# Performance work log

Measured on AMD Instinct MI355X. Metric: run time of the kernel, lower is better.

The kernel has to match this reference:

```python
import jax, jax.numpy as jnp
import numpy as np

N0, N1, N2 = 200000, 100000, 20000
E1, E2 = 1600000, 320000
D_IN, D_H, D_OUT = 128, 256, 64


def _segment_mean(vals, seg_ids, num_segments):
    # vals: [E, D], seg_ids: [E] int -> [num_segments, D] mean over incoming edges
    sums = jax.ops.segment_sum(vals, seg_ids, num_segments=num_segments)
    cnt = jax.ops.segment_sum(jnp.ones((vals.shape[0],), vals.dtype), seg_ids,
                              num_segments=num_segments)
    return sums / jnp.maximum(cnt, 1.0)[:, None]


def setup_inputs() -> dict:
    key = jax.random.key(0)
    ks = jax.random.split(key, 9)
    s = 1.0 / np.sqrt(D_IN)
    s2 = 1.0 / np.sqrt(D_H)
    return {
        "x": jax.random.normal(ks[0], (N0, D_IN), jnp.float32),
        "src1": jax.random.randint(ks[1], (E1,), 0, N0, jnp.int32),
        "dst1": jax.random.randint(ks[2], (E1,), 0, N1, jnp.int32),
        "src2": jax.random.randint(ks[3], (E2,), 0, N1, jnp.int32),
        "dst2": jax.random.randint(ks[4], (E2,), 0, N2, jnp.int32),
        "W_l1": jax.random.uniform(ks[5], (D_H, D_IN), jnp.float32, -s, s),
        "b_l1": jnp.zeros((D_H,), jnp.float32),
        "W_r1": jax.random.uniform(ks[6], (D_H, D_IN), jnp.float32, -s, s),
        "W_l2": jax.random.uniform(ks[7], (D_OUT, D_H), jnp.float32, -s2, s2),
        "b_l2": jnp.zeros((D_OUT,), jnp.float32),
        "W_r2": jax.random.uniform(ks[8], (D_OUT, D_H), jnp.float32, -s2, s2),
    }


def reference(x, src1, dst1, src2, dst2, W_l1, b_l1, W_r1, W_l2, b_l2, W_r2):
    # Layer 1: bipartite SAGEConv (N0 sources -> N1 targets), mean aggregation
    agg1 = _segment_mean(x[src1], dst1, N1)                    # [N1, D_IN]
    h1 = agg1 @ W_l1.T + b_l1 + x[:N1] @ W_r1.T                # [N1, D_H]
    h1 = jax.nn.relu(h1)                                       # dropout: eval no-op
    # Layer 2: (N1 -> N2)
    agg2 = _segment_mean(h1[src2], dst2, N2)                   # [N2, D_H]
    h2 = agg2 @ W_l2.T + b_l2 + h1[:N2] @ W_r2.T               # [N2, D_OUT]
    return jax.nn.log_softmax(h2, axis=-1)
```

## Files before the change

### kernel.cpp

```cpp
#include <hip/hip_runtime.h>
#include <hip/hip_fp8.h>
#include <stdint.h>


#define CN0 200000
#define CN1 100000
#define CN2 20000
#define CE1 1600000
#define CE2 320000
#define CD_IN 128
#define CD_H 256
#define CD_OUT 64

#define NBK1 196
#define NBK2 40
#define G1 256
#define G2 64
#define CHUNK1 6250
#define CHUNK2 5000

typedef __bf16 bf16x8 __attribute__((ext_vector_type(8)));
typedef float f32x2 __attribute__((ext_vector_type(2)));
typedef float f32x4 __attribute__((ext_vector_type(4)));
typedef float f32x16 __attribute__((ext_vector_type(16)));
typedef uint16_t u16x4 __attribute__((ext_vector_type(4)));

__device__ inline uint16_t f2bf(float f) {
  uint32_t u = __float_as_uint(f);
  return (uint16_t)((u + 0x7fffu + ((u >> 16) & 1u)) >> 16);
}
__device__ inline float blo(uint32_t v) { return __uint_as_float(v << 16); }
__device__ inline float bhi(uint32_t v) { return __uint_as_float(v & 0xffff0000u); }

__device__ inline uint32_t f32x4_to_fp8x4(float a, float b, float c, float d) {
#if __has_builtin(__builtin_amdgcn_cvt_pk_fp8_f32)
  uint32_t pk = (uint32_t)__builtin_amdgcn_cvt_pk_fp8_f32(a, b, 0, false);
  pk = (uint32_t)__builtin_amdgcn_cvt_pk_fp8_f32(c, d, (int)pk, true);
  return pk;
#else
  __hip_fp8_e4m3 e0(a), e1(b), e2(c), e3(d);
  return (uint32_t)e0.__x | ((uint32_t)e1.__x << 8) |
         ((uint32_t)e2.__x << 16) | ((uint32_t)e3.__x << 24);
#endif
}

__device__ inline float fp8_one(uint32_t b) {
  uint32_t s = (b >> 7) & 1u, e = (b >> 3) & 15u, m = b & 7u;
  float f = (e == 0) ? (float)m * 0.001953125f
                     : __uint_as_float(((e + 120u) << 23) | (m << 20));
  return s ? -f : f;
}

__device__ inline void fp8x4_dec(uint32_t w, float& p0, float& p1,
                                 float& p2, float& p3) {
#if __has_builtin(__builtin_amdgcn_cvt_pk_f32_fp8)
  f32x2 lo = __builtin_amdgcn_cvt_pk_f32_fp8(w, false);
  f32x2 hi = __builtin_amdgcn_cvt_pk_f32_fp8(w, true);
  p0 = lo[0]; p1 = lo[1]; p2 = hi[0]; p3 = hi[1];
#else
  p0 = fp8_one(w & 0xffu);
  p1 = fp8_one((w >> 8) & 0xffu);
  p2 = fp8_one((w >> 16) & 0xffu);
  p3 = fp8_one((w >> 24) & 0xffu);
#endif
}

__device__ inline void fp8x4_acc(uint32_t w, float& p0, float& p1,
                                 float& p2, float& p3) {
  float q0, q1, q2, q3;
  fp8x4_dec(w, q0, q1, q2, q3);
  p0 += q0; p1 += q1; p2 += q2; p3 += q3;
}

__device__ inline bf16x8 fp8x8_to_bf16x8(uint2 v) {
  float f[8];
  fp8x4_dec(v.x, f[0], f[1], f[2], f[3]);
  fp8x4_dec(v.y, f[4], f[5], f[6], f[7]);
  uint16_t o[8];
#pragma unroll
  for (int e = 0; e < 8; ++e) o[e] = f2bf(f[e]);
  return *reinterpret_cast<bf16x8*>(o);
}

__global__ __launch_bounds__(256) void cvt_count(
    const float* __restrict__ x, const float* __restrict__ Wl1,
    const float* __restrict__ Wr1, const float* __restrict__ Wl2,
    const float* __restrict__ Wr2, const int* __restrict__ dst1,
    const int* __restrict__ dst2, uint32_t* __restrict__ x_fp8,
    uint16_t* __restrict__ wfragG, uint16_t* __restrict__ w2fragG,
    int* __restrict__ H1, int* __restrict__ H2) {
  __shared__ int hist[256];
  int blk = blockIdx.x;
  if (blk < 12500) {
    int i = blk * 256 + threadIdx.x;
    const float4* xp = reinterpret_cast<const float4*>(x);
    float4 v0 = xp[2 * i];
    float4 v1 = xp[2 * i + 1];
    uint2 o;
    o.x = f32x4_to_fp8x4(v0.x, v0.y, v0.z, v0.w);
    o.y = f32x4_to_fp8x4(v1.x, v1.y, v1.z, v1.w);
    reinterpret_cast<uint2*>(x_fp8)[i] = o;
    return;
  }
  if (blk < 12548) {
    int c = (blk - 12500) * 256 + threadIdx.x;
    uint16_t o[8];
    if (c < 8192) {
      int lane = c & 63, t = (c >> 6) & 15, n = c >> 10;
      int row = n * 32 + (lane & 31);
      int kk = t * 16 + (lane >> 5) * 8;
      const float* srcp = (kk < 128) ? (Wl1 + (size_t)row * 128 + kk)
                                     : (Wr1 + (size_t)row * 128 + (kk - 128));
#pragma unroll
      for (int e = 0; e < 8; ++e) o[e] = f2bf(srcp[e]);
      *reinterpret_cast<int4*>(wfragG + (size_t)c * 8) = *reinterpret_cast<int4*>(o);
    } else {
      int cc = c - 8192;
      int lane = cc & 63, tt = (cc >> 6) & 15, j = cc >> 10;
      int row = j * 32 + (lane & 31);
      int kk = tt * 16 + (lane >> 5) * 8;
      const float* srcp = (row < 64) ? (Wl2 + (size_t)row * 256 + kk)
                                     : (Wr2 + (size_t)(row - 64) * 256 + kk);
#pragma unroll
      for (int e = 0; e < 8; ++e) o[e] = f2bf(srcp[e]);
      *reinterpret_cast<int4*>(w2fragG + (size_t)cc * 8) = *reinterpret_cast<int4*>(o);
    }
    return;
  }
  int g = blk - 12548, t = threadIdx.x;
  const int* dst; int* H; int E, nb, chunk;
  if (g < G1) { dst = dst1; H = H1; E = CE1; nb = NBK1; chunk = CHUNK1; }
  else { g -= G1; dst = dst2; H = H2; E = CE2; nb = NBK2; chunk = CHUNK2; }
  hist[t] = 0;
  __syncthreads();
  int e0 = g * chunk, e1 = min(e0 + chunk, E);
  for (int e = e0 + t; e < e1; e += 256) atomicAdd(&hist[dst[e] >> 9], 1);
  __syncthreads();
  if (t < nb) H[g * nb + t] = hist[t];
}

__global__ __launch_bounds__(256) void csr_scan(
    int* __restrict__ H1, int* __restrict__ H2,
    int* __restrict__ T1, int* __restrict__ T2) {
  __shared__ int sm[256];
  int b = blockIdx.x, t = threadIdx.x;
  int* H; int* T; int nb, G;
  if (b < NBK1) { H = H1; T = T1; nb = NBK1; G = G1; }
  else { b -= NBK1; H = H2; T = T2; nb = NBK2; G = G2; }
  int v = (t < G) ? H[t * nb + b] : 0;
  sm[t] = v;
  __syncthreads();
#pragma unroll
  for (int off = 1; off < 256; off <<= 1) {
    int u = (t >= off) ? sm[t - off] : 0;
    __syncthreads();
    sm[t] += u;
    __syncthreads();
  }
  if (t < G) H[t * nb + b] = sm[t] - v;
  if (t == 255) T[b] = sm[255];
}

__global__ __launch_bounds__(256) void csr_place(
    const int* __restrict__ src1, const int* __restrict__ dst1,
    const int* __restrict__ src2, const int* __restrict__ dst2,
    const int* __restrict__ H1, const int* __restrict__ H2,
    const int* __restrict__ T1, const int* __restrict__ T2,
    uint32_t* __restrict__ pairs1, uint32_t* __restrict__ pairs2) {
  __shared__ int curs[256];
  __shared__ int sm[256];
  int g = blockIdx.x, t = threadIdx.x;
  const int* src; const int* dst; const int* H; const int* T;
  uint32_t* pairs; int E, nb, chunk;
  if (g < G1) { src = src1; dst = dst1; H = H1; T = T1; pairs = pairs1;
                E = CE1; nb = NBK1; chunk = CHUNK1; }
  else { g -= G1; src = src2; dst = dst2; H = H2; T = T2; pairs = pairs2;
         E = CE2; nb = NBK2; chunk = CHUNK2; }
  int v = (t < nb) ? T[t] : 0;
  sm[t] = v;
  __syncthreads();
#pragma unroll
  for (int off = 1; off < 256; off <<= 1) {
    int u = (t >= off) ? sm[t - off] : 0;
    __syncthreads();
    sm[t] += u;
    __syncthreads();
  }
  if (t < nb) curs[t] = (sm[t] - v) + H[g * nb + t];
  __syncthreads();
  int e0 = g * chunk, e1 = min(e0 + chunk, E);
  for (int e = e0 + t; e < e1; e += 256) {
    int d = dst[e];
    int b = d >> 9;
    int p = atomicAdd(&curs[b], 1);
    pairs[p] = (uint32_t)src[e] | ((uint32_t)(d & 511) << 18);
  }
}

__global__ __launch_bounds__(256) void csr_bdeg_scan(
    const uint32_t* __restrict__ pairs1, const uint32_t* __restrict__ pairs2,
    const int* __restrict__ T1, const int* __restrict__ T2,
    int* __restrict__ deg1, int* __restrict__ deg2,
    int* __restrict__ R1, int* __restrict__ R2) {
  __shared__ int cnt[512];
  __shared__ int sm[256];
  int b = blockIdx.x, t = threadIdx.x;
  const uint32_t* pairs; const int* T;
  int* deg; int* R; int ndst;
  if (b < NBK1) { pairs = pairs1; T = T1; deg = deg1; R = R1; ndst = CN1; }
  else { b -= NBK1; pairs = pairs2; T = T2; deg = deg2; R = R2; ndst = CN2; }
  cnt[t] = 0;
  cnt[t + 256] = 0;
  sm[t] = (t < b) ? T[t] : 0;
  __syncthreads();
#pragma unroll
  for (int off = 128; off > 0; off >>= 1) {
    if (t < off) sm[t] += sm[t + off];
    __syncthreads();
  }
  int s0 = sm[0];
  int n = T[b];
  __syncthreads();
  for (int i = t; i < n; i += 256) atomicAdd(&cnt[pairs[s0 + i] >> 18], 1);
  __syncthreads();
  int d0 = b << 9;
  int a = cnt[2 * t], c = cnt[2 * t + 1];
  int i0 = d0 + 2 * t, i1 = d0 + 2 * t + 1;
  if (i0 < ndst) deg[i0] = a;
  if (i1 < ndst) deg[i1] = c;
  int s = a + c;
  sm[t] = s;
  __syncthreads();
#pragma unroll
  for (int off = 1; off < 256; off <<= 1) {
    int u = (t >= off) ? sm[t - off] : 0;
    __syncthreads();
    sm[t] += u;
    __syncthreads();
  }
  int excl = sm[t] - s;
  if (i0 < ndst) R[i0] = excl;
  if (i1 < ndst) R[i1] = excl + a;
}

__global__ __launch_bounds__(256) void csr_bplace(
    const uint32_t* __restrict__ pairs1, const uint32_t* __restrict__ pairs2,
    const int* __restrict__ T1, const int* __restrict__ T2,
    int* __restrict__ R1, int* __restrict__ R2,
    int* __restrict__ esrc1, int* __restrict__ esrc2) {
  __shared__ int cnt[512];
  __shared__ int sm[256];
  int b = blockIdx.x, t = threadIdx.x;
  const uint32_t* pairs; const int* T;
  int* R; int* esrc; int ndst;
  if (b < NBK1) { pairs = pairs1; T = T1; R = R1; esrc = esrc1; ndst = CN1; }
  else { b -= NBK1; pairs = pairs2; T = T2; R = R2; esrc = esrc2; ndst = CN2; }
  sm[t] = (t < b) ? T[t] : 0;
  __syncthreads();
#pragma unroll
  for (int off = 128; off > 0; off >>= 1) {
    if (t < off) sm[t] += sm[t + off];
    __syncthreads();
  }
  int s0 = sm[0];
  int n = T[b];
  __syncthreads();
  int d0 = b << 9;
#pragma unroll
  for (int j = 0; j < 2; ++j) {
    int dd = d0 + t + j * 256;
    if (dd < ndst) {
      int r = R[dd] + s0;
      cnt[t + j * 256] = r;
      R[dd] = r;
    } else {
      cnt[t + j * 256] = 0;
    }
  }
  __syncthreads();
  for (int i = t; i < n; i += 256) {
    uint32_t pk = pairs[s0 + i];
    int p = atomicAdd(&cnt[pk >> 18], 1);
    esrc[p] = (int)(pk & 0x3FFFFu);
  }
}

__global__ __launch_bounds__(256) void sage_gather1(
    const uint32_t* __restrict__ xf8, const int* __restrict__ esrc,
    const int* __restrict__ R, const int* __restrict__ deg,
    uint16_t* __restrict__ agg) {
  const int d = __builtin_amdgcn_readfirstlane(blockIdx.x * 4 + (threadIdx.x >> 6));
  const int lane = threadIdx.x & 63;
  const int cc = lane & 15;
  const int h = lane >> 4;
  const int start = __builtin_amdgcn_readfirstlane(R[d]);
  const int n = __builtin_amdgcn_readfirstlane(deg[d]);
  const uint2* xw = reinterpret_cast<const uint2*>(xf8);
  float a0 = 0.f, a1 = 0.f, a2 = 0.f, a3 = 0.f;
  float a4 = 0.f, a5 = 0.f, a6 = 0.f, a7 = 0.f;
  float c0 = 0.f, c1 = 0.f, c2 = 0.f, c3 = 0.f;
  float c4 = 0.f, c5 = 0.f, c6 = 0.f, c7 = 0.f;
  int i = 0;
  for (; i + 16 <= n; i += 16) {
    int s0 = esrc[start + i + h];
    int s1 = esrc[start + i + 4 + h];
    int s2 = esrc[start + i + 8 + h];
    int s3 = esrc[start + i + 12 + h];
    uint2 v0 = xw[(uint32_t)s0 * 16u + cc];
    uint2 v1 = xw[(uint32_t)s1 * 16u + cc];
    uint2 v2 = xw[(uint32_t)s2 * 16u + cc];
    uint2 v3 = xw[(uint32_t)s3 * 16u + cc];
    fp8x4_acc(v0.x, a0, a1, a2, a3);
    fp8x4_acc(v0.y, a4, a5, a6, a7);
    fp8x4_acc(v1.x, a0, a1, a2, a3);
    fp8x4_acc(v1.y, a4, a5, a6, a7);
    fp8x4_acc(v2.x, c0, c1, c2, c3);
    fp8x4_acc(v2.y, c4, c5, c6, c7);
    fp8x4_acc(v3.x, c0, c1, c2, c3);
    fp8x4_acc(v3.y, c4, c5, c6, c7);
  }
  for (; i + 4 <= n; i += 4) {
    int s0 = esrc[start + i + h];
    uint2 v = xw[(uint32_t)s0 * 16u + cc];
    fp8x4_acc(v.x, a0, a1, a2, a3);
    fp8x4_acc(v.y, a4, a5, a6, a7);
  }
  if (i < n && h < n - i) {
    int s0 = esrc[start + i + h];
    uint2 v = xw[(uint32_t)s0 * 16u + cc];
    fp8x4_acc(v.x, a0, a1, a2, a3);
    fp8x4_acc(v.y, a4, a5, a6, a7);
  }
  a0 += c0; a1 += c1; a2 += c2; a3 += c3;
  a4 += c4; a5 += c5; a6 += c6; a7 += c7;
  a0 += __shfl_xor(a0, 16); a0 += __shfl_xor(a0, 32);
  a1 += __shfl_xor(a1, 16); a1 += __shfl_xor(a1, 32);
  a2 += __shfl_xor(a2, 16); a2 += __shfl_xor(a2, 32);
  a3 += __shfl_xor(a3, 16); a3 += __shfl_xor(a3, 32);
  a4 += __shfl_xor(a4, 16); a4 += __shfl_xor(a4, 32);
  a5 += __shfl_xor(a5, 16); a5 += __shfl_xor(a5, 32);
  a6 += __shfl_xor(a6, 16); a6 += __shfl_xor(a6, 32);
  a7 += __shfl_xor(a7, 16); a7 += __shfl_xor(a7, 32);
  if (lane < 16) {
    float inv = 1.0f / fmaxf((float)n, 1.0f);
    uint4 o;
    o.x = (uint32_t)f2bf(a0 * inv) | ((uint32_t)f2bf(a1 * inv) << 16);
    o.y = (uint32_t)f2bf(a2 * inv) | ((uint32_t)f2bf(a3 * inv) << 16);
    o.z = (uint32_t)f2bf(a4 * inv) | ((uint32_t)f2bf(a5 * inv) << 16);
    o.w = (uint32_t)f2bf(a6 * inv) | ((uint32_t)f2bf(a7 * inv) << 16);
    reinterpret_cast<uint4*>(agg)[(size_t)d * 16 + cc] = o;
  }
}

__global__ __launch_bounds__(256) void sage_gather2_fin(
    const uint16_t* __restrict__ t2, const int* __restrict__ esrc,
    const int* __restrict__ R, const int* __restrict__ deg,
    const float* __restrict__ b2, float* __restrict__ out) {
  int d = blockIdx.x * 8 + (threadIdx.x >> 5);
  int c = threadIdx.x & 31;
  if (d >= CN2) return;
  int start = R[d], n = deg[d];
  const uint32_t* tw = reinterpret_cast<const uint32_t*>(t2);
  float a0 = 0.f, a1 = 0.f, b0 = 0.f, b1 = 0.f;
  int i = 0;
  for (; i + 8 <= n; i += 8) {
    int s0 = esrc[start + i + 0], s1 = esrc[start + i + 1];
    int s2 = esrc[start + i + 2], s3 = esrc[start + i + 3];
    int s4 = esrc[start + i + 4], s5 = esrc[start + i + 5];
    int s6 = esrc[start + i + 6], s7 = esrc[start + i + 7];
    uint32_t v0 = tw[(size_t)s0 * 32 + c], v1 = tw[(size_t)s1 * 32 + c];
    uint32_t v2 = tw[(size_t)s2 * 32 + c], v3 = tw[(size_t)s3 * 32 + c];
    uint32_t v4 = tw[(size_t)s4 * 32 + c], v5 = tw[(size_t)s5 * 32 + c];
    uint32_t v6 = tw[(size_t)s6 * 32 + c], v7 = tw[(size_t)s7 * 32 + c];
    a0 += (blo(v0) + blo(v1)) + (blo(v2) + blo(v3));
    b0 += (blo(v4) + blo(v5)) + (blo(v6) + blo(v7));
    a1 += (bhi(v0) + bhi(v1)) + (bhi(v2) + bhi(v3));
    b1 += (bhi(v4) + bhi(v5)) + (bhi(v6) + bhi(v7));
  }
  for (; i + 2 <= n; i += 2) {
    int s0 = esrc[start + i + 0], s1 = esrc[start + i + 1];
    uint32_t v0 = tw[(size_t)s0 * 32 + c], v1 = tw[(size_t)s1 * 32 + c];
    a0 += blo(v0) + blo(v1);
    a1 += bhi(v0) + bhi(v1);
  }
  if (i < n) {
    uint32_t v = tw[(size_t)esrc[start + i] * 32 + c];
    a0 += blo(v);
    a1 += bhi(v);
  }
  a0 += b0; a1 += b1;
  float inv = 1.0f / fmaxf((float)n, 1.0f);

  float2 ov = reinterpret_cast<const float2*>(out)[(size_t)d * 32 + c];
  float2 bb = reinterpret_cast<const float2*>(b2)[c];
  float v0 = ov.x + a0 * inv + bb.x;
  float v1 = ov.y + a1 * inv + bb.y;
  float m = fmaxf(v0, v1);
#pragma unroll
  for (int off = 16; off > 0; off >>= 1) m = fmaxf(m, __shfl_xor(m, off));
  float s = expf(v0 - m) + expf(v1 - m);
#pragma unroll
  for (int off = 16; off > 0; off >>= 1) s += __shfl_xor(s, off);
  float lg = logf(s);
  float2 r;
  r.x = v0 - m - lg;
  r.y = v1 - m - lg;
  reinterpret_cast<float2*>(out)[(size_t)d * 32 + c] = r;
}

__global__ __launch_bounds__(256, 2) void sage_mega(
    const uint16_t* __restrict__ agg, const uint32_t* __restrict__ xf8,
    const uint16_t* __restrict__ wfragG, const uint16_t* __restrict__ w2fragG,
    const float* __restrict__ bias, uint16_t* __restrict__ t2,
    float* __restrict__ outp) {
  __shared__ uint16_t wfrag[32768];
  __shared__ uint16_t h1t[4 * 32 * 40];
  const int tid = threadIdx.x;
  const int w = tid >> 6;
  const int lane = tid & 63;
  const int lcol = lane & 31;
  const int hi = lane >> 5;
  const int row0 = blockIdx.x * 128 + w * 32;
  uint16_t* hw = &h1t[w * (32 * 40)];

  int arow = row0 + lcol;
  arow = arow < CN1 ? arow : CN1 - 1;
  bf16x8 afr[16];
#pragma unroll
  for (int t = 0; t < 8; ++t) {
    afr[t] = *reinterpret_cast<const bf16x8*>(
        agg + (size_t)arow * CD_IN + t * 16 + hi * 8);
  }
#pragma unroll
  for (int t = 8; t < 16; ++t) {
    const int koff = t * 16 - 128;
    uint2 v = reinterpret_cast<const uint2*>(xf8)[
        (uint32_t)arow * 16u + (uint32_t)(koff >> 3) + (uint32_t)hi];
    afr[t] = fp8x8_to_bf16x8(v);
  }

  const bool do_out = (row0 < CN2);
  bf16x8 a2[16];

#pragma unroll
  for (int h = 0; h < 2; ++h) {
#pragma unroll
    for (int i = 0; i < 16; ++i) {
      int cc = i * 4 + w;
      int4 v = *reinterpret_cast<const int4*>(
          wfragG + (size_t)(h * 64 + cc) * 512 + lane * 8);
      *reinterpret_cast<int4*>(&wfrag[cc * 512 + lane * 8]) = v;
    }
    __syncthreads();
#pragma unroll
    for (int nn = 0; nn < 4; ++nn) {
      const int n = h * 4 + nn;
      const float bb = bias[n * 32 + lcol];
      f32x16 p0 = (f32x16)0.0f, p1 = (f32x16)0.0f;
#pragma unroll
      for (int t = 0; t < 16; t += 2) {
        bf16x8 b0 = *reinterpret_cast<const bf16x8*>(
            &wfrag[((nn * 16 + t) * 64 + lane) * 8]);
        bf16x8 b1 = *reinterpret_cast<const bf16x8*>(
            &wfrag[((nn * 16 + t + 1) * 64 + lane) * 8]);
        p0 = __builtin_amdgcn_mfma_f32_32x32x16_bf16(afr[t], b0, p0, 0, 0, 0);
        p1 = __builtin_amdgcn_mfma_f32_32x32x16_bf16(afr[t + 1], b1, p1, 0, 0, 0);
      }
#pragma unroll
      for (int r = 0; r < 16; ++r) {
        float v = fmaxf(p0[r] + p1[r] + bb, 0.0f);
        int R = (r & 3) + 8 * (r >> 2) + 4 * hi;
        hw[R * 40 + lcol] = f2bf(v);
      }
      a2[n * 2 + 0] = *reinterpret_cast<const bf16x8*>(&hw[lcol * 40 + hi * 8]);
      a2[n * 2 + 1] = *reinterpret_cast<const bf16x8*>(&hw[lcol * 40 + 16 + hi * 8]);
    }
    __syncthreads();
  }

#pragma unroll
  for (int i = 0; i < 16; ++i) {
    int cc = i * 4 + w;
    int4 v = *reinterpret_cast<const int4*>(
        w2fragG + (size_t)cc * 512 + lane * 8);
    *reinterpret_cast<int4*>(&wfrag[cc * 512 + lane * 8]) = v;
  }
  __syncthreads();

#pragma unroll
  for (int jp = 0; jp < 2; ++jp) {
    if (jp == 1 && !do_out) break;
    const int jA = jp * 2, jB = jp * 2 + 1;
    f32x16 aA = (f32x16)0.0f, aB = (f32x16)0.0f;
#pragma unroll
    for (int s = 0; s < 8; ++s) {
      bf16x8 c0A = *reinterpret_cast<const bf16x8*>(
          &wfrag[((jA * 16 + s * 2) * 64 + lane) * 8]);
      bf16x8 c1A = *reinterpret_cast<const bf16x8*>(
          &wfrag[((jA * 16 + s * 2 + 1) * 64 + lane) * 8]);
      bf16x8 c0B = *reinterpret_cast<const bf16x8*>(
          &wfrag[((jB * 16 + s * 2) * 64 + lane) * 8]);
      bf16x8 c1B = *reinterpret_cast<const bf16x8*>(
          &wfrag[((jB * 16 + s * 2 + 1) * 64 + lane) * 8]);
      aA = __builtin_amdgcn_mfma_f32_32x32x16_bf16(a2[s * 2], c0A, aA, 0, 0, 0);
      aB = __builtin_amdgcn_mfma_f32_32x32x16_bf16(a2[s * 2], c0B, aB, 0, 0, 0);
      aA = __builtin_amdgcn_mfma_f32_32x32x16_bf16(a2[s * 2 + 1], c1A, aA, 0, 0, 0);
      aB = __builtin_amdgcn_mfma_f32_32x32x16_bf16(a2[s * 2 + 1], c1B, aB, 0, 0, 0);
    }
    if (jp == 0) {
#pragma unroll
      for (int r = 0; r < 16; ++r) {
        int R = (r & 3) + 8 * (r >> 2) + 4 * hi;
        int rg = row0 + R;
        if (rg < CN1) {
          t2[(size_t)rg * 64 + lcol] = f2bf(aA[r]);
          t2[(size_t)rg * 64 + 32 + lcol] = f2bf(aB[r]);
        }
      }
    } else {
#pragma unroll
      for (int r = 0; r < 16; ++r) {
        int R = (r & 3) + 8 * (r >> 2) + 4 * hi;
        int rg = row0 + R;
        outp[(size_t)rg * 64 + lcol] = aA[r];
        outp[(size_t)rg * 64 + 32 + lcol] = aB[r];
      }
    }
  }
}

extern "C" void kernel_launch(void* const* d_in, const int* in_sizes, int n_in,
                              void* d_out, int out_size, void* d_ws, size_t ws_size,
                              hipStream_t stream) {
  const float* x    = (const float*)d_in[0];
  const int* src1   = (const int*)d_in[1];
  const int* dst1   = (const int*)d_in[2];
  const int* src2   = (const int*)d_in[3];
  const int* dst2   = (const int*)d_in[4];
  const float* W_l1 = (const float*)d_in[5];
  const float* b_l1 = (const float*)d_in[6];
  const float* W_r1 = (const float*)d_in[7];
  const float* W_l2 = (const float*)d_in[8];
  const float* b_l2 = (const float*)d_in[9];
  const float* W_r2 = (const float*)d_in[10];
  float* out = (float*)d_out;
  char* base = (char*)d_ws;

  uint32_t* x_fp8 = (uint32_t*)base;
  uint16_t* t2_bf = (uint16_t*)(base + 25600000);
  uint16_t* agg_bf= (uint16_t*)(base + 38400000);
  uint32_t* pairs1= (uint32_t*)(base + 38400000);
  uint32_t* pairs2= (uint32_t*)(base + 44800000);
  int* deg1 = (int*)(base + 64000000);
  int* R1   = (int*)(base + 64400000);
  int* esrc1= (int*)(base + 64800000);
  int* deg2 = (int*)(base + 71200000);
  int* R2   = (int*)(base + 71280000);
  int* esrc2= (int*)(base + 71360000);
  int* H1   = (int*)(base + 72640000);
  int* H2   = (int*)(base + 72840704);
  char* misc = base + 72850944;
  int* T1  = (int*)(misc);
  int* T2  = (int*)(misc + 2048);
  uint16_t* wfragG  = (uint16_t*)(misc + 6144);
  uint16_t* w2fragG = wfragG + 65536;

  if (ws_size < 74000000u) return;

  cvt_count<<<12868, 256, 0, stream>>>(x, W_l1, W_r1, W_l2, W_r2, dst1, dst2,
                                       x_fp8, wfragG, w2fragG, H1, H2);

  csr_scan<<<NBK1 + NBK2, 256, 0, stream>>>(H1, H2, T1, T2);
  csr_place<<<G1 + G2, 256, 0, stream>>>(src1, dst1, src2, dst2, H1, H2,
                                         T1, T2, pairs1, pairs2);
  csr_bdeg_scan<<<NBK1 + NBK2, 256, 0, stream>>>(pairs1, pairs2, T1, T2,
                                                 deg1, deg2, R1, R2);
  csr_bplace<<<NBK1 + NBK2, 256, 0, stream>>>(pairs1, pairs2, T1, T2,
                                              R1, R2, esrc1, esrc2);

  sage_gather1<<<(CN1 + 3) / 4, 256, 0, stream>>>(x_fp8, esrc1, R1, deg1, agg_bf);
  sage_mega<<<(CN1 + 127) / 128, 256, 0, stream>>>(
      agg_bf, x_fp8, wfragG, w2fragG, b_l1, t2_bf, out);
  sage_gather2_fin<<<(CN2 + 7) / 8, 256, 0, stream>>>(
      t2_bf, esrc2, R2, deg2, b_l2, out);
}
```

Before: 169.8 us.

## Double-buffer weight fragments in LDS and prefetch next chunk during MFMA

Splits the 64 KB LDS weight buffer into two 32 KB halves. Each next chunk of layer-1 or layer-2 weights is loaded into registers while the MFMAs on the current chunk run, then written to the other half before the barrier. This hides global weight-load latency behind compute and drops from two big load-then-sync phases to four smaller pipelined ones. s_setprio is raised around the MFMA loops. The cost is 8 extra int4 staging registers per thread, which could add register pressure under launch_bounds(256,2).

```diff
diff --git a/kernel.cpp b/kernel.cpp
--- a/kernel.cpp
+++ b/kernel.cpp
@@ -422,6 +422,8 @@
   const int hi = lane >> 5;
   const int row0 = blockIdx.x * 128 + w * 32;
   uint16_t* hw = &h1t[w * (32 * 40)];
+  uint16_t* buf0 = wfrag;
+  uint16_t* buf1 = wfrag + 16384;
 
   int arow = row0 + lcol;
   arow = arow < CN1 ? arow : CN1 - 1;
@@ -441,31 +443,55 @@
 
   const bool do_out = (row0 < CN2);
   bf16x8 a2[16];
-
-#pragma unroll
-  for (int h = 0; h < 2; ++h) {
-#pragma unroll
-    for (int i = 0; i < 16; ++i) {
-      int cc = i * 4 + w;
-      int4 v = *reinterpret_cast<const int4*>(
-          wfragG + (size_t)(h * 64 + cc) * 512 + lane * 8);
-      *reinterpret_cast<int4*>(&wfrag[cc * 512 + lane * 8]) = v;
-    }
-    __syncthreads();
-#pragma unroll
-    for (int nn = 0; nn < 4; ++nn) {
-      const int n = h * 4 + nn;
+  int4 st[8];
+
+#pragma unroll
+  for (int i = 0; i < 8; ++i) {
+    int cc = i * 4 + w;
+    st[i] = *reinterpret_cast<const int4*>(wfragG + (size_t)cc * 512 + lane * 8);
+  }
+#pragma unroll
+  for (int i = 0; i < 8; ++i) {
+    int cc = i * 4 + w;
+    *reinterpret_cast<int4*>(&buf0[cc * 512 + lane * 8]) = st[i];
+  }
+  __syncthreads();
+
+#pragma unroll
+  for (int q = 0; q < 4; ++q) {
+    uint16_t* cur = (q & 1) ? buf1 : buf0;
+    uint16_t* nxt = (q & 1) ? buf0 : buf1;
+    if (q < 3) {
+#pragma unroll
+      for (int i = 0; i < 8; ++i) {
+        int cc = i * 4 + w;
+        st[i] = *reinterpret_cast<const int4*>(
+            wfragG + (size_t)((q + 1) * 32 + cc) * 512 + lane * 8);
+      }
+    } else {
+#pragma unroll
+      for (int i = 0; i < 8; ++i) {
+        int cc = i * 4 + w;
+        st[i] = *reinterpret_cast<const int4*>(
+            w2fragG + (size_t)cc * 512 + lane * 8);
+      }
+    }
+#pragma unroll
+    for (int nq = 0; nq < 2; ++nq) {
+      const int n = q * 2 + nq;
       const float bb = bias[n * 32 + lcol];
       f32x16 p0 = (f32x16)0.0f, p1 = (f32x16)0.0f;
+      __builtin_amdgcn_s_setprio(1);
 #pragma unroll
       for (int t = 0; t < 16; t += 2) {
         bf16x8 b0 = *reinterpret_cast<const bf16x8*>(
-            &wfrag[((nn * 16 + t) * 64 + lane) * 8]);
+            &cur[((nq * 16 + t) * 64 + lane) * 8]);
         bf16x8 b1 = *reinterpret_cast<const bf16x8*>(
-            &wfrag[((nn * 16 + t + 1) * 64 + lane) * 8]);
+            &cur[((nq * 16 + t + 1) * 64 + lane) * 8]);
         p0 = __builtin_amdgcn_mfma_f32_32x32x16_bf16(afr[t], b0, p0, 0, 0, 0);
         p1 = __builtin_amdgcn_mfma_f32_32x32x16_bf16(afr[t + 1], b1, p1, 0, 0, 0);
       }
+      __builtin_amdgcn_s_setprio(0);
 #pragma unroll
       for (int r = 0; r < 16; ++r) {
         float v = fmaxf(p0[r] + p1[r] + bb, 0.0f);
@@ -475,56 +501,80 @@
       a2[n * 2 + 0] = *reinterpret_cast<const bf16x8*>(&hw[lcol * 40 + hi * 8]);
       a2[n * 2 + 1] = *reinterpret_cast<const bf16x8*>(&hw[lcol * 40 + 16 + hi * 8]);
     }
-    __syncthreads();
-  }
-
-#pragma unroll
-  for (int i = 0; i < 16; ++i) {
+#pragma unroll
+    for (int i = 0; i < 8; ++i) {
+      int cc = i * 4 + w;
+      *reinterpret_cast<int4*>(&nxt[cc * 512 + lane * 8]) = st[i];
+    }
+    __syncthreads();
+  }
+
+#pragma unroll
+  for (int i = 0; i < 8; ++i) {
     int cc = i * 4 + w;
-    int4 v = *reinterpret_cast<const int4*>(
-        w2fragG + (size_t)cc * 512 + lane * 8);
-    *reinterpret_cast<int4*>(&wfrag[cc * 512 + lane * 8]) = v;
-  }
-  __syncthreads();
-
-#pragma unroll
-  for (int jp = 0; jp < 2; ++jp) {
-    if (jp == 1 && !do_out) break;
-    const int jA = jp * 2, jB = jp * 2 + 1;
+    st[i] = *reinterpret_cast<const int4*>(
+        w2fragG + (size_t)(32 + cc) * 512 + lane * 8);
+  }
+  {
     f32x16 aA = (f32x16)0.0f, aB = (f32x16)0.0f;
+    __builtin_amdgcn_s_setprio(1);
 #pragma unroll
     for (int s = 0; s < 8; ++s) {
       bf16x8 c0A = *reinterpret_cast<const bf16x8*>(
-          &wfrag[((jA * 16 + s * 2) * 64 + lane) * 8]);
+          &buf0[((0 * 16 + s * 2) * 64 + lane) * 8]);
       bf16x8 c1A = *reinterpret_cast<const bf16x8*>(
-          &wfrag[((jA * 16 + s * 2 + 1) * 64 + lane) * 8]);
+          &buf0[((0 * 16 + s * 2 + 1) * 64 + lane) * 8]);
       bf16x8 c0B = *reinterpret_cast<const bf16x8*>(
-          &wfrag[((jB * 16 + s * 2) * 64 + lane) * 8]);
+          &buf0[((1 * 16 + s * 2) * 64 + lane) * 8]);
       bf16x8 c1B = *reinterpret_cast<const bf16x8*>(
-          &wfrag[((jB * 16 + s * 2 + 1) * 64 + lane) * 8]);
+          &buf0[((1 * 16 + s * 2 + 1) * 64 + lane) * 8]);
       aA = __builtin_amdgcn_mfma_f32_32x32x16_bf16(a2[s * 2], c0A, aA, 0, 0, 0);
       aB = __builtin_amdgcn_mfma_f32_32x32x16_bf16(a2[s * 2], c0B, aB, 0, 0, 0);
       aA = __builtin_amdgcn_mfma_f32_32x32x16_bf16(a2[s * 2 + 1], c1A, aA, 0, 0, 0);
       aB = __builtin_amdgcn_mfma_f32_32x32x16_bf16(a2[s * 2 + 1], c1B, aB, 0, 0, 0);
     }
-    if (jp == 0) {
-#pragma unroll
-      for (int r = 0; r < 16; ++r) {
-        int R = (r & 3) + 8 * (r >> 2) + 4 * hi;
-        int rg = row0 + R;
-        if (rg < CN1) {
-          t2[(size_t)rg * 64 + lcol] = f2bf(aA[r]);
-          t2[(size_t)rg * 64 + 32 + lcol] = f2bf(aB[r]);
-        }
+    __builtin_amdgcn_s_setprio(0);
+#pragma unroll
+    for (int r = 0; r < 16; ++r) {
+      int R = (r & 3) + 8 * (r >> 2) + 4 * hi;
+      int rg = row0 + R;
+      if (rg < CN1) {
+        t2[(size_t)rg * 64 + lcol] = f2bf(aA[r]);
+        t2[(size_t)rg * 64 + 32 + lcol] = f2bf(aB[r]);
       }
-    } else {
-#pragma unroll
-      for (int r = 0; r < 16; ++r) {
-        int R = (r & 3) + 8 * (r >> 2) + 4 * hi;
-        int rg = row0 + R;
-        outp[(size_t)rg * 64 + lcol] = aA[r];
-        outp[(size_t)rg * 64 + 32 + lcol] = aB[r];
-      }
+    }
+  }
+#pragma unroll
+  for (int i = 0; i < 8; ++i) {
+    int cc = i * 4 + w;
+    *reinterpret_cast<int4*>(&buf1[cc * 512 + lane * 8]) = st[i];
+  }
+  __syncthreads();
+  if (do_out) {
+    f32x16 aA = (f32x16)0.0f, aB = (f32x16)0.0f;
+    __builtin_amdgcn_s_setprio(1);
+#pragma unroll
+    for (int s = 0; s < 8; ++s) {
+      bf16x8 c0A = *reinterpret_cast<const bf16x8*>(
+          &buf1[((0 * 16 + s * 2) * 64 + lane) * 8]);
+      bf16x8 c1A = *reinterpret_cast<const bf16x8*>(
+          &buf1[((0 * 16 + s * 2 + 1) * 64 + lane) * 8]);
+      bf16x8 c0B = *reinterpret_cast<const bf16x8*>(
+          &buf1[((1 * 16 + s * 2) * 64 + lane) * 8]);
+      bf16x8 c1B = *reinterpret_cast<const bf16x8*>(
+          &buf1[((1 * 16 + s * 2 + 1) * 64 + lane) * 8]);
+      aA = __builtin_amdgcn_mfma_f32_32x32x16_bf16(a2[s * 2], c0A, aA, 0, 0, 0);
+      aB = __builtin_amdgcn_mfma_f32_32x32x16_bf16(a2[s * 2], c0B, aB, 0, 0, 0);
+      aA = __builtin_amdgcn_mfma_f32_32x32x16_bf16(a2[s * 2 + 1], c1A, aA, 0, 0, 0);
+      aB = __builtin_amdgcn_mfma_f32_32x32x16_bf16(a2[s * 2 + 1], c1B, aB, 0, 0, 0);
+    }
+    __builtin_amdgcn_s_setprio(0);
+#pragma unroll
+    for (int r = 0; r < 16; ++r) {
+      int R = (r & 3) + 8 * (r >> 2) + 4 * hi;
+      int rg = row0 + R;
+      outp[(size_t)rg * 64 + lcol] = aA[r];
+      outp[(size_t)rg * 64 + 32 + lcol] = aB[r];
     }
   }
 }
```

Measured after the change: 170.8 us. Within noise of the previous version (+0.6%).
